# Optimization experiments

Hardware: AMD Instinct MI355X
Metric: run time of the kernel (lower is better)

The kernel has to match this reference:

```python
import jax, jax.numpy as jnp
import numpy as np

NUM_HEADS = 8
HEAD_DIM = 16
NEG_SLOPE = 0.2


def setup_inputs() -> dict:
    key = jax.random.key(0)
    k1, k2, k3, k4, k5 = jax.random.split(key, 5)
    N, E, D_IN, D_OUT = 100000, 1600000, 128, 128
    x = jax.random.normal(k1, (N, D_IN), dtype=jnp.float32)
    edge_indices = jax.random.randint(k2, (2, E), 0, N, dtype=jnp.int64)
    W = jax.random.normal(k3, (D_OUT, D_IN), dtype=jnp.float32) * (1.0 / np.sqrt(D_IN))
    src_attn = jax.random.normal(k4, (1, NUM_HEADS, HEAD_DIM), dtype=jnp.float32) * (1.0 / np.sqrt(HEAD_DIM))
    dst_attn = jax.random.normal(k5, (1, NUM_HEADS, HEAD_DIM), dtype=jnp.float32) * (1.0 / np.sqrt(HEAD_DIM))
    return {"x": x, "edge_indices": edge_indices, "W": W, "src_attn": src_attn, "dst_attn": dst_attn}


def reference(x, edge_indices, W, src_attn, dst_attn):
    N = x.shape[0]
    # add self loops (i, i) for every node
    loops = jnp.arange(N, dtype=edge_indices.dtype)
    ei = jnp.concatenate([edge_indices, jnp.stack([loops, loops])], axis=1)  # [2, E+N]
    row, col = ei[0], ei[1]

    # linear projection + head split: [N, H, hd]
    h = (x @ W.T).reshape(N, NUM_HEADS, HEAD_DIM)

    # per-node attention logits, gathered per edge: [E', H]
    s = jnp.sum(h * src_attn, axis=-1)  # [N, H]
    d = jnp.sum(h * dst_attn, axis=-1)  # [N, H]
    e = jax.nn.leaky_relu(s[row] + d[col], negative_slope=NEG_SLOPE)  # [E', H]

    # sparse softmax over each row's neighborhood (dim=1 of the sparse matrix)
    m = jax.ops.segment_max(e, row, num_segments=N)  # [N, H]
    e = jnp.exp(e - m[row])
    z = jax.ops.segment_sum(e, row, num_segments=N)  # [N, H]
    a = e / z[row]  # [E', H]

    # per-head SpMM: out[row] += a * h[col]
    out = jax.ops.segment_sum(a[:, :, None] * h[col], row, num_segments=N)  # [N, H, hd]
    return out.reshape(N, NUM_HEADS * HEAD_DIM)
```

## Files before the change

kernel.cpp:

```cpp
#include <hip/hip_runtime.h>
#include <hip/hip_bf16.h>
#include <math.h>

#define NEG_SLOPE 0.2f

typedef __attribute__((ext_vector_type(8))) short short8v;
typedef __attribute__((ext_vector_type(4))) float f32x4;

__global__ __launch_bounds__(256) void gat_prep(
    const float* __restrict__ W, const float* __restrict__ srcA,
    const float* __restrict__ dstA, ushort* __restrict__ wbf,
    int* __restrict__ count, int N)
{
  for (int i = blockIdx.x * 256 + threadIdx.x; i < N; i += gridDim.x * 256)
    count[i] = 0;

  int tid = blockIdx.x * 256 + threadIdx.x;
  if (tid >= 36 * 64) return;
  int frag = tid >> 6, lane = tid & 63;
  int nt = frag >> 2, ks = frag & 3;
  int kbase = ks * 32 + (lane >> 4) * 8;
  ushort v[8];
  if (nt < 8) {
    int r = nt * 16 + (lane & 15);
#pragma unroll
    for (int j = 0; j < 8; ++j)
      v[j] = __bfloat16_as_ushort(__float2bfloat16(W[(size_t)r * 128 + kbase + j]));
  } else {
    int n = lane & 15;
    int hd = n & 7;
    const float* av = (n < 8) ? srcA : dstA;
#pragma unroll
    for (int j = 0; j < 8; ++j) {
      float acc = 0.f;
      int k = kbase + j;
      for (int d = 0; d < 16; ++d)
        acc += W[(size_t)(hd * 16 + d) * 128 + k] * av[hd * 16 + d];
      v[j] = __bfloat16_as_ushort(__float2bfloat16(acc));
    }
  }
  ushort* dst = wbf + ((size_t)frag * 64 + lane) * 8;
#pragma unroll
  for (int j = 0; j < 8; ++j) dst[j] = v[j];
}

__global__ __launch_bounds__(256, 2) void gat_gemm_hist(
    const float* __restrict__ x, const ushort* __restrict__ wbf,
    ushort* __restrict__ hb, float* __restrict__ s, float* __restrict__ dv,
    int N, int nchunks, int G1,
    const int* __restrict__ ei, int E, int* __restrict__ count,
    int* __restrict__ rank, int userank)
{
  const int q = (int)blockIdx.x / 5;
  const int r5 = (int)blockIdx.x % 5;
  if (r5 == 0) {
    const int wave = threadIdx.x >> 6, lane = threadIdx.x & 63;
    const int lrow = lane & 15, lkg = lane >> 4;

    short8v b[36];
    const short8v* wv = (const short8v*)wbf;
#pragma unroll
    for (int f = 0; f < 36; ++f) b[f] = wv[(size_t)f * 64 + lane];

    for (int chunk = q; chunk < nchunks; chunk += G1) {
      const int r0 = chunk * 64 + wave * 16;
      int arow = r0 + lrow; if (arow > N - 1) arow = N - 1;
      const float* xr = x + (size_t)arow * 128 + lkg * 8;

      f32x4 acc[9];
#pragma unroll
      for (int t = 0; t < 9; ++t) acc[t] = (f32x4){0.f, 0.f, 0.f, 0.f};

#pragma unroll
      for (int ks = 0; ks < 4; ++ks) {
        float4 x0 = *(const float4*)(xr + ks * 32);
        float4 x1 = *(const float4*)(xr + ks * 32 + 4);
        short8v a;
        a[0] = (short)__bfloat16_as_ushort(__float2bfloat16(x0.x));
        a[1] = (short)__bfloat16_as_ushort(__float2bfloat16(x0.y));
        a[2] = (short)__bfloat16_as_ushort(__float2bfloat16(x0.z));
        a[3] = (short)__bfloat16_as_ushort(__float2bfloat16(x0.w));
        a[4] = (short)__bfloat16_as_ushort(__float2bfloat16(x1.x));
        a[5] = (short)__bfloat16_as_ushort(__float2bfloat16(x1.y));
        a[6] = (short)__bfloat16_as_ushort(__float2bfloat16(x1.z));
        a[7] = (short)__bfloat16_as_ushort(__float2bfloat16(x1.w));
#pragma unroll
        for (int t = 0; t < 9; ++t)
          acc[t] = __builtin_amdgcn_mfma_f32_16x16x32_bf16(a, b[t * 4 + ks], acc[t], 0, 0, 0);
      }

      const int rbase = r0 + lkg * 4;
#pragma unroll
      for (int t = 0; t < 8; ++t) {
#pragma unroll
        for (int r = 0; r < 4; ++r) {
          int row = rbase + r;
          if (row < N)
            hb[(size_t)row * 128 + t * 16 + lrow] =
                __bfloat16_as_ushort(__float2bfloat16(acc[t][r]));
        }
      }
#pragma unroll
      for (int r = 0; r < 4; ++r) {
        int row = rbase + r;
        if (row < N) {
          if (lrow < 8) s[(size_t)row * 8 + lrow] = acc[8][r];
          else          dv[(size_t)row * 8 + (lrow - 8)] = acc[8][r];
        }
      }
    }
  } else {
    __shared__ int sh64;
    if (threadIdx.x == 0) sh64 = 1;
    __syncthreads();
    if (ei[2 * threadIdx.x + 1] != 0) sh64 = 0;
    __syncthreads();
    const int is64 = sh64;

    const int hb_id = q * 4 + (r5 - 1);
    const int nhb = 4 * G1;
    int i = hb_id * 256 + threadIdx.x;
    const int stride = nhb * 256;
    for (; i < E; i += stride) {
      int r = is64 ? ei[2 * i] : ei[i];
      int old = atomicAdd(&count[r], 1);
      if (userank) rank[i] = old;
    }
  }
}

__global__ __launch_bounds__(256) void gat_scan_part(
    const int* __restrict__ count, int N, int* __restrict__ partial)
{
  __shared__ int sm[256];
  int base = blockIdx.x * 1024;
  int tsum = 0;
  for (int i = threadIdx.x; i < 1024; i += 256) {
    int idx = base + i;
    if (idx < N) tsum += count[idx] + 1;
  }
  sm[threadIdx.x] = tsum;
  __syncthreads();
  for (int off = 128; off > 0; off >>= 1) {
    if (threadIdx.x < off) sm[threadIdx.x] += sm[threadIdx.x + off];
    __syncthreads();
  }
  if (threadIdx.x == 0) partial[blockIdx.x] = sm[0];
}

__global__ __launch_bounds__(1024) void gat_scan_mid(int* __restrict__ partial, int nb)
{
  __shared__ int sm[1024];
  int t = threadIdx.x;
  int v = (t < nb) ? partial[t] : 0;
  sm[t] = v;
  __syncthreads();
  int acc = v;
  for (int off = 1; off < 1024; off <<= 1) {
    int other = (t >= off) ? sm[t - off] : 0;
    __syncthreads();
    acc += other;
    sm[t] = acc;
    __syncthreads();
  }
  if (t < nb) partial[t] = acc - v;
}

__global__ __launch_bounds__(256) void gat_scan_final(
    const int* __restrict__ count, int N, const int* __restrict__ partial,
    int* __restrict__ offsets, int* __restrict__ cursor, int total)
{
  __shared__ int sm[256];
  int base = blockIdx.x * 1024 + threadIdx.x * 4;
  int v[4];
  int tsum = 0;
#pragma unroll
  for (int j = 0; j < 4; ++j) {
    int idx = base + j;
    v[j] = (idx < N) ? (count[idx] + 1) : 0;
    tsum += v[j];
  }
  sm[threadIdx.x] = tsum;
  __syncthreads();
  int acc = tsum;
  for (int off = 1; off < 256; off <<= 1) {
    int other = (threadIdx.x >= off) ? sm[threadIdx.x - off] : 0;
    __syncthreads();
    acc += other;
    sm[threadIdx.x] = acc;
    __syncthreads();
  }
  int ex = acc - tsum + partial[blockIdx.x];
#pragma unroll
  for (int j = 0; j < 4; ++j) {
    int idx = base + j;
    if (idx < N) { offsets[idx] = ex; cursor[idx] = ex; ex += v[j]; }
  }
  if (blockIdx.x == 0 && threadIdx.x == 0) offsets[N] = total;
}

__global__ __launch_bounds__(256) void gat_scatter_rank(
    const int* __restrict__ ei, int E, int N,
    const int* __restrict__ offsets, const int* __restrict__ count,
    const int* __restrict__ rank, int* __restrict__ scol)
{
  __shared__ int sh64;
  if (threadIdx.x == 0) sh64 = 1;
  __syncthreads();
  if (ei[2 * threadIdx.x + 1] != 0) sh64 = 0;
  __syncthreads();
  const int is64 = sh64;

  int i = blockIdx.x * 256 + threadIdx.x;
  const int stride = gridDim.x * 256;
  const int total = E + N;
  for (; i < total; i += stride) {
    int pos, c;
    if (i < E) {
      int r;
      if (is64) { r = ei[2 * i]; c = ei[2 * (E + i)]; }
      else      { r = ei[i];     c = ei[E + i]; }
      pos = offsets[r] + rank[i];
    } else {
      int r = i - E; c = r;
      pos = offsets[r] + count[r];
    }
    scol[pos] = c;
  }
}

__global__ __launch_bounds__(256) void gat_scatter(
    const int* __restrict__ ei, int E, int N,
    int* __restrict__ cursor, int* __restrict__ scol)
{
  __shared__ int sh64;
  if (threadIdx.x == 0) sh64 = 1;
  __syncthreads();
  if (ei[2 * threadIdx.x + 1] != 0) sh64 = 0;
  __syncthreads();
  const int is64 = sh64;

  int i = blockIdx.x * 256 + threadIdx.x;
  const int stride = gridDim.x * 256;
  const int total = E + N;
  for (; i < total; i += stride) {
    int r, c;
    if (i < E) {
      if (is64) { r = ei[2 * i]; c = ei[2 * (E + i)]; }
      else      { r = ei[i];     c = ei[E + i]; }
    } else {
      r = i - E; c = r;
    }
    int pos = atomicAdd(&cursor[r], 1);
    scol[pos] = c;
  }
}

__global__ __launch_bounds__(256) void gat_agg(
    const uint* __restrict__ hb, const float* __restrict__ s, const float* __restrict__ dv,
    const int* __restrict__ offsets, const int* __restrict__ scol,
    float* __restrict__ out, int N)
{
  int wid = (int)((blockIdx.x * 256 + threadIdx.x) >> 6);
  int lane = threadIdx.x & 63;
  if (wid >= N) return;
  const int g = lane >> 4;
  const int t = lane & 15;
  const int head = t >> 1;
  const int beg = __builtin_amdgcn_readfirstlane(offsets[wid]);
  const int end = __builtin_amdgcn_readfirstlane(offsets[wid + 1]);
  const float sl = s[wid * 8 + head];

  const char* hbp = (const char*)hb;
  const char* dvp = (const char*)dv;
  const uint hoff = (uint)t * 16u;
  const uint doff = (uint)head * 4u;

  float z = 0.f;
  float a0 = 0, a1 = 0, a2 = 0, a3 = 0, a4 = 0, a5 = 0, a6 = 0, a7 = 0;

  const int nq = (end - beg + 3) >> 2;
  const int lasti = end - 1;

  int iA = beg + g;       iA = iA < end ? iA : lasti;
  int iB = beg + 4 + g;   iB = iB < end ? iB : lasti;
  int iC = beg + 8 + g;   iC = iC < end ? iC : lasti;
  int cB = scol[iB];
  int cC = scol[iC];
  int cA = scol[iA];
  float dlA = *(const float*)(dvp + ((uint)cA * 32u + doff));
  uint4 huA = *(const uint4*)(hbp + ((uint)cA * 256u + hoff));
  float dlB = *(const float*)(dvp + ((uint)cB * 32u + doff));
  uint4 huB = *(const uint4*)(hbp + ((uint)cB * 256u + hoff));

  for (int j = 0; j < nq; ++j) {
    int iD = beg + 4 * (j + 3) + g; iD = iD < end ? iD : lasti;
    int cD = scol[iD];
    float dlC = *(const float*)(dvp + ((uint)cC * 32u + doff));
    uint4 huC = *(const uint4*)(hbp + ((uint)cC * 256u + hoff));

    float e = sl + dlA;
    e = fmaxf(e, NEG_SLOPE * e);
    float w = (beg + 4 * j + g < end) ? __expf(e) : 0.f;
    z += w;
    a0 = fmaf(w, __uint_as_float(huA.x << 16), a0);
    a1 = fmaf(w, __uint_as_float(huA.x & 0xFFFF0000u), a1);
    a2 = fmaf(w, __uint_as_float(huA.y << 16), a2);
    a3 = fmaf(w, __uint_as_float(huA.y & 0xFFFF0000u), a3);
    a4 = fmaf(w, __uint_as_float(huA.z << 16), a4);
    a5 = fmaf(w, __uint_as_float(huA.z & 0xFFFF0000u), a5);
    a6 = fmaf(w, __uint_as_float(huA.w << 16), a6);
    a7 = fmaf(w, __uint_as_float(huA.w & 0xFFFF0000u), a7);

    dlA = dlB; huA = huB;
    dlB = dlC; huB = huC;
    cC = cD;
  }

  a0 += __shfl_xor(a0, 16, 64); a0 += __shfl_xor(a0, 32, 64);
  a1 += __shfl_xor(a1, 16, 64); a1 += __shfl_xor(a1, 32, 64);
  a2 += __shfl_xor(a2, 16, 64); a2 += __shfl_xor(a2, 32, 64);
  a3 += __shfl_xor(a3, 16, 64); a3 += __shfl_xor(a3, 32, 64);
  a4 += __shfl_xor(a4, 16, 64); a4 += __shfl_xor(a4, 32, 64);
  a5 += __shfl_xor(a5, 16, 64); a5 += __shfl_xor(a5, 32, 64);
  a6 += __shfl_xor(a6, 16, 64); a6 += __shfl_xor(a6, 32, 64);
  a7 += __shfl_xor(a7, 16, 64); a7 += __shfl_xor(a7, 32, 64);
  z  += __shfl_xor(z, 16, 64);  z  += __shfl_xor(z, 32, 64);

  float inv = 1.f / z;
  if (lane < 16) {
    float4* op = (float4*)(out + (size_t)wid * 128 + t * 8);
    op[0] = make_float4(a0 * inv, a1 * inv, a2 * inv, a3 * inv);
    op[1] = make_float4(a4 * inv, a5 * inv, a6 * inv, a7 * inv);
  }
}

extern "C" void kernel_launch(void* const* d_in, const int* in_sizes, int n_in,
                              void* d_out, int out_size, void* d_ws, size_t ws_size,
                              hipStream_t stream) {
  const float* x    = (const float*)d_in[0];
  const int*   ei   = (const int*)d_in[1];
  const float* W    = (const float*)d_in[2];
  const float* srcA = (const float*)d_in[3];
  const float* dstA = (const float*)d_in[4];
  float* out = (float*)d_out;
  const int N = in_sizes[0] / 128;
  const int E = in_sizes[1] / 2;

  ushort* hbuf = (ushort*)d_ws;
  float* s  = (float*)(hbuf + (size_t)N * 128);
  float* dv = s + (size_t)N * 8;
  ushort* wbf = (ushort*)(dv + (size_t)N * 8);
  int* count   = (int*)((char*)wbf + 36864);
  int* offsets = count + N;
  int* cursor  = offsets + (N + 1);
  int* partial = cursor + N;
  int* scol    = partial + 1024;
  int* rank    = scol + (E + N);

  const size_t need_rank = (size_t)((char*)(rank + E) - (char*)d_ws);
  const int userank = (ws_size >= need_rank) ? 1 : 0;

  const int nchunks = (N + 63) / 64;
  const int G1 = 512;

  gat_prep<<<2048, 256, 0, stream>>>(W, srcA, dstA, wbf, count, N);
  gat_gemm_hist<<<5 * G1, 256, 0, stream>>>(x, wbf, hbuf, s, dv, N, nchunks, G1,
                                            ei, E, count, rank, userank);
  const int nb = (N + 1023) / 1024;
  gat_scan_part<<<nb, 256, 0, stream>>>(count, N, partial);
  gat_scan_mid<<<1, 1024, 0, stream>>>(partial, nb);
  gat_scan_final<<<nb, 256, 0, stream>>>(count, N, partial, offsets, cursor, E + N);
  if (userank)
    gat_scatter_rank<<<2048, 256, 0, stream>>>(ei, E, N, offsets, count, rank, scol);
  else
    gat_scatter<<<2048, 256, 0, stream>>>(ei, E, N, cursor, scol);
  gat_agg<<<(N + 3) / 4, 256, 0, stream>>>((const uint*)hbuf, s, dv, offsets, scol, out, N);
}
```

Before: 202.4 us.

## Replace three-kernel scan with single-pass decoupled-lookback scan; split aggregation launch

The three scan kernels (partial sums, middle scan, final scan) are merged into one kernel that takes block ids from a ticket and uses decoupled lookback over per-block state words to get the exclusive prefix. This drops two kernel launches and the extra pass over the counts. The state array and ticket are zeroed in the prep kernel. The aggregation kernel now takes a row range and is launched twice over the two halves of the nodes, which adds a launch without an obvious benefit. The lookback spin loop depends on the 256-entry state array covering every block (nb is about 98 here).

```diff
diff --git a/kernel.cpp b/kernel.cpp
--- a/kernel.cpp
+++ b/kernel.cpp
@@ -10,14 +10,17 @@
 __global__ __launch_bounds__(256) void gat_prep(
     const float* __restrict__ W, const float* __restrict__ srcA,
     const float* __restrict__ dstA, ushort* __restrict__ wbf,
-    int* __restrict__ count, int N)
-{
-  for (int i = blockIdx.x * 256 + threadIdx.x; i < N; i += gridDim.x * 256)
+    int* __restrict__ count, int N,
+    unsigned int* __restrict__ state, int* __restrict__ ticket)
+{
+  int gtid = blockIdx.x * 256 + threadIdx.x;
+  for (int i = gtid; i < N; i += gridDim.x * 256)
     count[i] = 0;
-
-  int tid = blockIdx.x * 256 + threadIdx.x;
-  if (tid >= 36 * 64) return;
-  int frag = tid >> 6, lane = tid & 63;
+  if (gtid < 256) state[gtid] = 0;
+  if (gtid == 0) *ticket = 0;
+
+  if (gtid >= 36 * 64) return;
+  int frag = gtid >> 6, lane = gtid & 63;
   int nt = frag >> 2, ks = frag & 3;
   int kbase = ks * 32 + (lane >> 4) * 8;
   ushort v[8];
@@ -129,57 +132,26 @@
   }
 }
 
-__global__ __launch_bounds__(256) void gat_scan_part(
-    const int* __restrict__ count, int N, int* __restrict__ partial)
-{
+__global__ __launch_bounds__(256) void gat_scan(
+    const int* __restrict__ count, int N, int nb,
+    unsigned int* __restrict__ state, int* __restrict__ ticket,
+    int* __restrict__ offsets, int* __restrict__ cursor, int total)
+{
+  __shared__ int sbid;
   __shared__ int sm[256];
-  int base = blockIdx.x * 1024;
-  int tsum = 0;
-  for (int i = threadIdx.x; i < 1024; i += 256) {
-    int idx = base + i;
-    if (idx < N) tsum += count[idx] + 1;
-  }
-  sm[threadIdx.x] = tsum;
-  __syncthreads();
-  for (int off = 128; off > 0; off >>= 1) {
-    if (threadIdx.x < off) sm[threadIdx.x] += sm[threadIdx.x + off];
-    __syncthreads();
-  }
-  if (threadIdx.x == 0) partial[blockIdx.x] = sm[0];
-}
-
-__global__ __launch_bounds__(1024) void gat_scan_mid(int* __restrict__ partial, int nb)
-{
-  __shared__ int sm[1024];
-  int t = threadIdx.x;
-  int v = (t < nb) ? partial[t] : 0;
-  sm[t] = v;
-  __syncthreads();
-  int acc = v;
-  for (int off = 1; off < 1024; off <<= 1) {
-    int other = (t >= off) ? sm[t - off] : 0;
-    __syncthreads();
-    acc += other;
-    sm[t] = acc;
-    __syncthreads();
-  }
-  if (t < nb) partial[t] = acc - v;
-}
-
-__global__ __launch_bounds__(256) void gat_scan_final(
-    const int* __restrict__ count, int N, const int* __restrict__ partial,
-    int* __restrict__ offsets, int* __restrict__ cursor, int total)
-{
-  __shared__ int sm[256];
-  int base = blockIdx.x * 1024 + threadIdx.x * 4;
-  int v[4];
-  int tsum = 0;
-#pragma unroll
-  for (int j = 0; j < 4; ++j) {
-    int idx = base + j;
-    v[j] = (idx < N) ? (count[idx] + 1) : 0;
-    tsum += v[j];
-  }
+  __shared__ int sprefix;
+  if (threadIdx.x == 0) sbid = atomicAdd(ticket, 1);
+  __syncthreads();
+  const int bid = sbid;
+  const int base = bid * 1024 + threadIdx.x * 4;
+
+  int v0 = 0, v1 = 0, v2 = 0, v3 = 0;
+  if (base + 0 < N) v0 = count[base + 0] + 1;
+  if (base + 1 < N) v1 = count[base + 1] + 1;
+  if (base + 2 < N) v2 = count[base + 2] + 1;
+  if (base + 3 < N) v3 = count[base + 3] + 1;
+  int tsum = v0 + v1 + v2 + v3;
+
   sm[threadIdx.x] = tsum;
   __syncthreads();
   int acc = tsum;
@@ -190,13 +162,33 @@
     sm[threadIdx.x] = acc;
     __syncthreads();
   }
-  int ex = acc - tsum + partial[blockIdx.x];
-#pragma unroll
-  for (int j = 0; j < 4; ++j) {
-    int idx = base + j;
-    if (idx < N) { offsets[idx] = ex; cursor[idx] = ex; ex += v[j]; }
-  }
-  if (blockIdx.x == 0 && threadIdx.x == 0) offsets[N] = total;
+  const int blocktotal = sm[255];
+
+  if (threadIdx.x == 0) {
+    __hip_atomic_store(&state[bid], (1u << 30) | (unsigned)blocktotal,
+                       __ATOMIC_RELEASE, __HIP_MEMORY_SCOPE_AGENT);
+    int ex = 0;
+    int j = bid - 1;
+    while (j >= 0) {
+      unsigned d = __hip_atomic_load(&state[j], __ATOMIC_ACQUIRE, __HIP_MEMORY_SCOPE_AGENT);
+      unsigned st = d >> 30;
+      if (st == 0u) continue;
+      ex += (int)(d & 0x3FFFFFFFu);
+      if (st >= 2u) break;
+      --j;
+    }
+    __hip_atomic_store(&state[bid], (2u << 30) | (unsigned)(ex + blocktotal),
+                       __ATOMIC_RELEASE, __HIP_MEMORY_SCOPE_AGENT);
+    sprefix = ex;
+  }
+  __syncthreads();
+
+  int e = sprefix + acc - tsum;
+  if (base + 0 < N) { offsets[base + 0] = e; cursor[base + 0] = e; e += v0; }
+  if (base + 1 < N) { offsets[base + 1] = e; cursor[base + 1] = e; e += v1; }
+  if (base + 2 < N) { offsets[base + 2] = e; cursor[base + 2] = e; e += v2; }
+  if (base + 3 < N) { offsets[base + 3] = e; cursor[base + 3] = e; e += v3; }
+  if (bid == nb - 1 && threadIdx.x == 255) offsets[N] = total;
 }
 
 __global__ __launch_bounds__(256) void gat_scatter_rank(
@@ -259,11 +251,11 @@
 __global__ __launch_bounds__(256) void gat_agg(
     const uint* __restrict__ hb, const float* __restrict__ s, const float* __restrict__ dv,
     const int* __restrict__ offsets, const int* __restrict__ scol,
-    float* __restrict__ out, int N)
-{
-  int wid = (int)((blockIdx.x * 256 + threadIdx.x) >> 6);
+    float* __restrict__ out, int rowbase, int rowlim)
+{
+  int wid = rowbase + (int)((blockIdx.x * 256 + threadIdx.x) >> 6);
   int lane = threadIdx.x & 63;
-  if (wid >= N) return;
+  if (wid >= rowlim) return;
   const int g = lane >> 4;
   const int t = lane & 15;
   const int head = t >> 1;
@@ -354,8 +346,9 @@
   int* count   = (int*)((char*)wbf + 36864);
   int* offsets = count + N;
   int* cursor  = offsets + (N + 1);
-  int* partial = cursor + N;
-  int* scol    = partial + 1024;
+  unsigned int* state = (unsigned int*)(cursor + N);
+  int* ticket  = (int*)(state + 256);
+  int* scol    = ticket + 4;
   int* rank    = scol + (E + N);
 
   const size_t need_rank = (size_t)((char*)(rank + E) - (char*)d_ws);
@@ -364,16 +357,16 @@
   const int nchunks = (N + 63) / 64;
   const int G1 = 512;
 
-  gat_prep<<<2048, 256, 0, stream>>>(W, srcA, dstA, wbf, count, N);
+  gat_prep<<<2048, 256, 0, stream>>>(W, srcA, dstA, wbf, count, N, state, ticket);
   gat_gemm_hist<<<5 * G1, 256, 0, stream>>>(x, wbf, hbuf, s, dv, N, nchunks, G1,
                                             ei, E, count, rank, userank);
   const int nb = (N + 1023) / 1024;
-  gat_scan_part<<<nb, 256, 0, stream>>>(count, N, partial);
-  gat_scan_mid<<<1, 1024, 0, stream>>>(partial, nb);
-  gat_scan_final<<<nb, 256, 0, stream>>>(count, N, partial, offsets, cursor, E + N);
+  gat_scan<<<nb, 256, 0, stream>>>(count, N, nb, state, ticket, offsets, cursor, E + N);
   if (userank)
     gat_scatter_rank<<<2048, 256, 0, stream>>>(ei, E, N, offsets, count, rank, scol);
   else
     gat_scatter<<<2048, 256, 0, stream>>>(ei, E, N, cursor, scol);
-  gat_agg<<<(N + 3) / 4, 256, 0, stream>>>((const uint*)hbuf, s, dv, offsets, scol, out, N);
-}
+  const int half = N / 2;
+  gat_agg<<<(half + 3) / 4, 256, 0, stream>>>((const uint*)hbuf, s, dv, offsets, scol, out, 0, half);
+  gat_agg<<<(N - half + 3) / 4, 256, 0, stream>>>((const uint*)hbuf, s, dv, offsets, scol, out, half, N);
+}
```

Measured after the change: 225.3 us. +11.3%, slower.
